# Kernel tuning notes

Hardware: AMD Instinct MI355X
Metric: run time of the kernel (lower is better)

The kernel has to match this reference:

```python
import jax, jax.numpy as jnp
import numpy as np

E = 8        # num_experts
K = 2        # top_k
LN_EPS = 1e-5

def setup_inputs() -> dict:
    key = jax.random.key(0)
    B, S, D, F = 4, 2048, 1024, 4096
    F2 = F // 2  # shared expert ffn_dim // 2
    ks = jax.random.split(key, 8)
    s = 0.02
    return {
        "hidden_states": jax.random.normal(ks[0], (B, S, D), jnp.float32),
        "router_w": jax.random.normal(ks[1], (D, E), jnp.float32) * s,
        "router_b": jnp.zeros((E,), jnp.float32),
        "w1": jax.random.normal(ks[2], (E, D, F), jnp.float32) * s,
        "b1": jnp.zeros((E, F), jnp.float32),
        "gate": jnp.ones((E, F), jnp.float32),          # specialization_gate per expert
        "w2": jax.random.normal(ks[3], (E, F, D), jnp.float32) * s,
        "b2": jnp.zeros((E, D), jnp.float32),
        "sw1": jax.random.normal(ks[4], (D, F2), jnp.float32) * s,
        "sb1": jnp.zeros((F2,), jnp.float32),
        "sgate": jnp.ones((F2,), jnp.float32),
        "sw2": jax.random.normal(ks[5], (F2, D), jnp.float32) * s,
        "sb2": jnp.zeros((D,), jnp.float32),
        "shared_weight": jnp.float32(0.5),
        "ln_g": jnp.ones((D,), jnp.float32),
        "ln_b": jnp.zeros((D,), jnp.float32),
    }


def _expert_ffn(x, w1, b1, gate, w2, b2):
    # fc1 -> specialization gate -> exact GELU -> fc2 (dropout is identity in eval)
    h = jax.nn.gelu((x @ w1 + b1) * gate, approximate=False)
    return h @ w2 + b2


def reference(hidden_states, router_w, router_b, w1, b1, gate, w2, b2,
              sw1, sb1, sgate, sw2, sb2, shared_weight, ln_g, ln_b):
    x = hidden_states  # [B,S,D]
    # --- router (eval: no noise, no capacity mask) ---
    logits = jnp.einsum('bsd,de->bse', x, router_w) + router_b
    probs = jax.nn.softmax(logits, axis=-1)                # [B,S,E]
    topk_p, topk_i = jax.lax.top_k(probs, K)               # [B,S,K]
    topk_p = topk_p / jnp.sum(topk_p, axis=-1, keepdims=True)
    # per-token per-expert combine weight: sum over k slots assigned to expert e
    combine = jnp.sum(jax.nn.one_hot(topk_i, E, dtype=x.dtype) * topk_p[..., None], axis=-2)  # [B,S,E]
    # --- expert dispatch/combine (dense equivalent; zero weight = no contribution) ---
    moe = jnp.zeros_like(x)
    for e in range(E):  # small fixed loop over experts
        moe = moe + combine[..., e:e + 1] * _expert_ffn(x, w1[e], b1[e], gate[e], w2[e], b2[e])
    # --- shared expert ---
    shared = _expert_ffn(x, sw1, sb1, sgate, sw2, sb2) * jax.nn.sigmoid(shared_weight)
    y = moe + shared
    # --- output LayerNorm ---
    mu = jnp.mean(y, axis=-1, keepdims=True)
    var = jnp.var(y, axis=-1, keepdims=True)
    return (y - mu) * jax.lax.rsqrt(var + LN_EPS) * ln_g + ln_b
```

## Files before the change

kernel.cpp:

```cpp
#include <hip/hip_runtime.h>
#include <hip/hip_bf16.h>
#include <stdint.h>

typedef __attribute__((ext_vector_type(8))) short bf16x8;
typedef __attribute__((ext_vector_type(4))) float f32x4;
typedef __attribute__((ext_vector_type(4))) unsigned short us4;

#define T_TOK 8192
#define DDIM 1024
#define FDIM 4096
#define F2DIM 2048
#define NEXP 8
#define NTPB1 4352
#define NRBLK 2048
#define FC1_T 5344

__device__ __forceinline__ unsigned short f2bf(float f) {
    unsigned u = __float_as_uint(f);
    u += 0x7fffu + ((u >> 16) & 1u);
    return (unsigned short)(u >> 16);
}
__device__ __forceinline__ float bf2f(unsigned short h) {
    return __uint_as_float(((unsigned)h) << 16);
}
__device__ __forceinline__ float gelu_fast(float v) {
    float u = 0.7978845608028654f * v * (1.0f + 0.044715f * v * v);
    float a = fabsf(u);
    float t = __expf(-2.0f * a);
    float th = (1.0f - t) / (1.0f + t);
    th = u < 0.0f ? -th : th;
    return 0.5f * v * (1.0f + th);
}

__device__ __forceinline__ void gl2lds16(const void* g, void* l) {
    __builtin_amdgcn_global_load_lds(
        (const __attribute__((address_space(1))) unsigned int*)(unsigned long long)g,
        (__attribute__((address_space(3))) unsigned int*)(unsigned int)(unsigned long long)l,
        16, 0, 0);
}

__device__ __forceinline__ void tp_block(const float* __restrict__ in,
                                         unsigned short* __restrict__ out,
                                         int Cin, long long ibase, int n0, int k0,
                                         long long unit0, float (*ts)[132], int tid) {
#pragma unroll
    for (int i = 0; i < 8; ++i) {
        int idx = tid + i * 256;
        int k = idx >> 5, t4 = idx & 31;
        float4 v = *(const float4*)(in + ibase + (long long)(k0 + k) * Cin + n0 + t4 * 4);
        *(float4*)&ts[k][t4 * 4] = v;
    }
    __syncthreads();
#pragma unroll
    for (int i = 0; i < 4; ++i) {
        int idx = tid + i * 256;
        int u = idx >> 9, cid = idx & 511;
        int row = cid >> 2, c = cid & 3;
        int gc = c ^ ((row >> 1) & 3);
        const int kb = u * 32 + gc * 8;
        us4 o0, o1;
        o0.x = f2bf(ts[kb + 0][row]); o0.y = f2bf(ts[kb + 1][row]);
        o0.z = f2bf(ts[kb + 2][row]); o0.w = f2bf(ts[kb + 3][row]);
        o1.x = f2bf(ts[kb + 4][row]); o1.y = f2bf(ts[kb + 5][row]);
        o1.z = f2bf(ts[kb + 6][row]); o1.w = f2bf(ts[kb + 7][row]);
        unsigned short* dst = out + (unit0 + u) * 4096 + (long long)cid * 8;
        *(us4*)dst = o0;
        *(us4*)(dst + 4) = o1;
    }
}

__global__ void k_prep1(const float* __restrict__ w1, const float* __restrict__ sw1,
                        unsigned short* __restrict__ w1t, unsigned short* __restrict__ sw1t,
                        const float* __restrict__ x, const float* __restrict__ rw,
                        const float* __restrict__ rbv, int* __restrict__ eid,
                        float* __restrict__ ewt, int* __restrict__ bcnt,
                        unsigned short* __restrict__ xb) {
    const int blk = blockIdx.x;
    const int tid = threadIdx.x;

    if (blk < NTPB1) {
        __shared__ float ts[64][132];
        if (blk < 4096) {
            int e = blk >> 9, l = blk & 511;
            int nb = l >> 4, ks = l & 15;
            tp_block(w1, w1t, 4096, (long long)e * 1024 * 4096,
                     nb * 128, ks * 64, (long long)e * 1024 + nb * 32 + ks * 2, ts, tid);
        } else {
            int l = blk - 4096;
            int nb = l >> 4, ks = l & 15;
            tp_block(sw1, sw1t, 2048, 0, nb * 128, ks * 64, nb * 32 + ks * 2, ts, tid);
        }
        return;
    }

    __shared__ int hcnt[8];
    const int rblk = blk - NTPB1;
    const int wid = tid >> 6, lane = tid & 63;
    const int t = rblk * 4 + wid;
    if (tid < 8) hcnt[tid] = 0;
    __syncthreads();

    float acc[8];
#pragma unroll
    for (int e = 0; e < 8; ++e) acc[e] = 0.f;
    const float4* xr = (const float4*)(x + (long long)t * DDIM);
#pragma unroll
    for (int c = 0; c < 4; ++c) {
        float4 xv = xr[lane + 64 * c];
        int d0 = (lane + 64 * c) * 4;
        us4 o;
        o.x = f2bf(xv.x); o.y = f2bf(xv.y); o.z = f2bf(xv.z); o.w = f2bf(xv.w);
        *(us4*)(xb + (long long)t * DDIM + d0) = o;
        float xs[4] = {xv.x, xv.y, xv.z, xv.w};
#pragma unroll
        for (int j = 0; j < 4; ++j) {
            const float* wrow = rw + (long long)(d0 + j) * 8;
#pragma unroll
            for (int e = 0; e < 8; ++e) acc[e] += xs[j] * wrow[e];
        }
    }
#pragma unroll
    for (int off = 32; off; off >>= 1)
#pragma unroll
        for (int e = 0; e < 8; ++e) acc[e] += __shfl_xor(acc[e], off);
    if (lane == 0) {
        float lg[8];
#pragma unroll
        for (int e = 0; e < 8; ++e) lg[e] = acc[e] + rbv[e];
        int e0 = 0;
#pragma unroll
        for (int e = 1; e < 8; ++e) if (lg[e] > lg[e0]) e0 = e;
        int e1 = -1;
#pragma unroll
        for (int e = 0; e < 8; ++e) {
            if (e == e0) continue;
            if (e1 < 0 || lg[e] > lg[e1]) e1 = e;
        }
        float w0 = 1.f / (1.f + expf(lg[e1] - lg[e0]));
        eid[2 * t] = e0; eid[2 * t + 1] = e1;
        ewt[2 * t] = w0; ewt[2 * t + 1] = 1.f - w0;
        atomicAdd(&hcnt[e0], 1);
        atomicAdd(&hcnt[e1], 1);
    }
    __syncthreads();
    if (tid < 8) bcnt[rblk * 8 + tid] = hcnt[tid];
}

__global__ void k_scan2(const int* __restrict__ bcnt, int* __restrict__ cnt,
                        int* __restrict__ offs, int* __restrict__ blkbase) {
    __shared__ int part[256];
    __shared__ int ctot[8];
    __shared__ int gbase[8];
    const int tid = threadIdx.x;
    const int e = tid >> 5, j = tid & 31;
    int s = 0;
    for (int r = j * 64; r < j * 64 + 64; ++r) s += bcnt[r * 8 + e];
    part[tid] = s;
    __syncthreads();
    if (j == 0) {
        int run = 0;
        for (int k = 0; k < 32; ++k) { int v = part[e * 32 + k]; part[e * 32 + k] = run; run += v; }
        ctot[e] = run;
    }
    __syncthreads();
    if (tid == 0) {
        int run = 0;
        for (int ee = 0; ee < NEXP; ++ee) {
            offs[ee] = run; cnt[ee] = ctot[ee]; gbase[ee] = run; run += ctot[ee];
        }
        offs[NEXP] = run;
    }
    __syncthreads();
    int run = gbase[e] + part[tid];
    for (int r = j * 64; r < j * 64 + 64; ++r) {
        blkbase[r * 8 + e] = run;
        run += bcnt[r * 8 + e];
    }
}

__global__ void k_scatter2(const int* __restrict__ eid, const float* __restrict__ ewt,
                           const int* __restrict__ blkbase, int* __restrict__ rowtok,
                           float* __restrict__ roww, int* __restrict__ pos) {
    const int t = blockIdx.x * 256 + threadIdx.x;
    const int rb = t >> 2;
    const int g = t & 3;
    const int lane = threadIdx.x & 63;
    const int lb = lane & ~3;
    int e0 = eid[2 * t], e1 = eid[2 * t + 1];
    int r0 = 0, r1 = 0;
#pragma unroll
    for (int q = 0; q < 4; ++q) {
        int oe0 = __shfl(e0, lb + q, 64);
        int oe1 = __shfl(e1, lb + q, 64);
        if (q < g) {
            r0 += (oe0 == e0) + (oe1 == e0);
            r1 += (oe0 == e1) + (oe1 == e1);
        }
    }
    int p0 = blkbase[rb * 8 + e0] + r0;
    int p1 = blkbase[rb * 8 + e1] + r1;
    rowtok[p0] = (t << 1);     roww[p0] = ewt[2 * t];     pos[2 * t] = p0;
    rowtok[p1] = (t << 1) | 1; roww[p1] = ewt[2 * t + 1]; pos[2 * t + 1] = p1;
}

template <int FC>
__launch_bounds__(256, 4)
__global__ void k_fc(const short* __restrict__ Amoe, const short* __restrict__ Ash,
                     const short* __restrict__ Bmoe, const short* __restrict__ Bsh,
                     const float* __restrict__ biasM, const float* __restrict__ biasS,
                     const float* __restrict__ gateM, const float* __restrict__ gateS,
                     unsigned short* __restrict__ outM, unsigned short* __restrict__ outS,
                     const int* __restrict__ cnt, const int* __restrict__ offs,
                     const int* __restrict__ rowtok, const float* __restrict__ roww,
                     const float* __restrict__ swp,
                     const float* __restrict__ w2raw, const float* __restrict__ sw2raw,
                     unsigned short* __restrict__ w2t_o, unsigned short* __restrict__ sw2t_o) {
    __shared__ __align__(16) char smem_raw[34816];

    if (FC == 1 && blockIdx.x >= FC1_T) {
        float (*ts)[132] = (float(*)[132])smem_raw;
        int tb = blockIdx.x - FC1_T;
        if (tb < 4096) {
            int e = tb >> 9, l = tb & 511;
            int nb = l >> 6, ks = l & 63;
            tp_block(w2raw, w2t_o, 1024, (long long)e * 4096 * 1024,
                     nb * 128, ks * 64, (long long)e * 1024 + nb * 128 + ks * 2,
                     ts, threadIdx.x);
        } else {
            int l = tb - 4096;
            int nb = l >> 5, ks = l & 31;
            tp_block(sw2raw, sw2t_o, 1024, 0, nb * 128, ks * 64,
                     nb * 64 + ks * 2, ts, threadIdx.x);
        }
        return;
    }

    int RBz[9];
    int T = 0;
#pragma unroll
    for (int zz = 0; zz < 9; ++zz) {
        int Mz = (zz < 8) ? cnt[zz] : T_TOK;
        int rbn = (Mz + 127) >> 7;
        int cbn = (FC == 1) ? ((zz < 8) ? 32 : 16) : 8;
        RBz[zz] = rbn;
        T += rbn * cbn;
    }
    const int ell = blockIdx.x;
    if (ell >= T) return;
    const int q = T >> 3, r = T & 7;
    const int xk = ell & 7, jj = ell >> 3;
    int t = (xk < r ? xk * (q + 1) : r * (q + 1) + (xk - r) * q) + jj;

    int z = 0, local = t;
    for (; z < 9; ++z) {
        int cbn = (FC == 1) ? ((z < 8) ? 32 : 16) : 8;
        int tz = RBz[z] * cbn;
        if (local < tz) break;
        local -= tz;
    }
    const int RB = RBz[z];
    int cb, rb;
    if (FC == 1) {
        cb = local / RB;
        rb = local - cb * RB;
    } else {
        rb = local >> 3;
        cb = local & 7;
    }

    const bool sh = (z == 8);
    const int Kd = (FC == 1) ? 1024 : (sh ? 2048 : 4096);
    const int Ncols = (FC == 1) ? (sh ? 2048 : 4096) : 1024;
    const int KB = Kd / 32;
    const int M = sh ? T_TOK : cnt[z];
    const int oE = sh ? 0 : offs[z];

    const short* A = sh ? Ash : Amoe;
    const short* B = sh ? Bsh : Bmoe + (long long)z * 4194304;

    short* Asb = (short*)smem_raw;
    short* Bsb = Asb + 8192;

    const int tid = threadIdx.x, w = tid >> 6, lane = tid & 63;
    const int fr = lane & 15, fg = lane >> 4;
    const int wr = w >> 1, wc = w & 1;

    const short *ag0, *ag1;
    {
        int id = tid, row = id >> 2;
        int gc = (id & 3) ^ ((row >> 1) & 3);
        int rA = rb * 128 + row; if (rA > M - 1) rA = M - 1;
        long long rowix;
        if (FC == 1) rowix = sh ? (long long)rA : (long long)(rowtok[oE + rA] >> 1);
        else         rowix = sh ? (long long)rA : (long long)(oE + rA);
        ag0 = A + rowix * (long long)Kd + gc * 8;
    }
    {
        int id = tid + 256, row = id >> 2;
        int gc = (id & 3) ^ ((row >> 1) & 3);
        int rA = rb * 128 + row; if (rA > M - 1) rA = M - 1;
        long long rowix;
        if (FC == 1) rowix = sh ? (long long)rA : (long long)(rowtok[oE + rA] >> 1);
        else         rowix = sh ? (long long)rA : (long long)(oE + rA);
        ag1 = A + rowix * (long long)Kd + gc * 8;
    }
    const short* bb = B + (long long)cb * KB * 4096 + (long long)tid * 8;

    short* const a0d0 = Asb + w * 512;
    short* const a0d1 = Asb + 2048 + w * 512;
    short* const a1d0 = Asb + 4096 + w * 512;
    short* const a1d1 = Asb + 4096 + 2048 + w * 512;
    short* const b0d0 = Bsb + w * 512;
    short* const b0d1 = Bsb + 2048 + w * 512;
    short* const b1d0 = Bsb + 4096 + w * 512;
    short* const b1d1 = Bsb + 4096 + 2048 + w * 512;

    f32x4 acc[4][4];
#pragma unroll
    for (int m = 0; m < 4; ++m)
#pragma unroll
        for (int n = 0; n < 4; ++n)
            acc[m][n] = (f32x4){0.f, 0.f, 0.f, 0.f};

    const int slot = fg ^ ((fr >> 1) & 3);
    const int arow0 = wr * 64 + fr;
    const int brow0 = wc * 64 + fr;
    const int nk = Kd / 64;

    for (int kt = 0; kt < nk; ++kt) {
        gl2lds16(ag0, a0d0);       gl2lds16(ag0 + 32, a1d0);
        gl2lds16(ag1, a0d1);       gl2lds16(ag1 + 32, a1d1);
        gl2lds16(bb, b0d0);        gl2lds16(bb + 2048, b0d1);
        gl2lds16(bb + 4096, b1d0); gl2lds16(bb + 6144, b1d1);
        ag0 += 64; ag1 += 64; bb += 8192;
        __syncthreads();

#pragma unroll
        for (int s = 0; s < 2; ++s) {
            bf16x8 a[4], b[4];
#pragma unroll
            for (int m = 0; m < 4; ++m)
                a[m] = *(const bf16x8*)(Asb + s * 4096 + (arow0 + m * 16) * 32 + slot * 8);
#pragma unroll
            for (int n = 0; n < 4; ++n)
                b[n] = *(const bf16x8*)(Bsb + s * 4096 + (brow0 + n * 16) * 32 + slot * 8);
#pragma unroll
            for (int m = 0; m < 4; ++m)
#pragma unroll
                for (int n = 0; n < 4; ++n)
                    acc[m][n] = __builtin_amdgcn_mfma_f32_16x16x32_bf16(a[m], b[n], acc[m][n], 0, 0, 0);
        }
        __syncthreads();
    }

    const int mrow0 = rb * 128 + wr * 64;
    const int col0 = cb * 128 + wc * 64;

    if (FC == 1) {
        const float* bp = sh ? biasS : biasM + (long long)z * FDIM;
        const float* gp = sh ? gateS : gateM + (long long)z * FDIM;
        unsigned short* outp = sh ? outS : outM;
        const long long obase = sh ? 0 : (long long)oE;
        float bv[4], gv[4]; int coln[4];
#pragma unroll
        for (int n = 0; n < 4; ++n) {
            coln[n] = col0 + n * 16 + fr;
            bv[n] = bp[coln[n]];
            gv[n] = gp[coln[n]];
        }
#pragma unroll
        for (int m = 0; m < 4; ++m) {
#pragma unroll
            for (int i = 0; i < 4; ++i) {
                int grow = mrow0 + m * 16 + fg * 4 + i;
                if (grow < M) {
                    unsigned short* rowp = outp + (obase + grow) * (long long)Ncols;
#pragma unroll
                    for (int n = 0; n < 4; ++n) {
                        float v = (acc[m][n][i] + bv[n]) * gv[n];
                        rowp[coln[n]] = f2bf(gelu_fast(v));
                    }
                }
            }
        }
    } else {
        float bv[4]; int coln[4];
        const float* bp = sh ? biasS : biasM + (long long)z * DDIM;
#pragma unroll
        for (int n = 0; n < 4; ++n) {
            coln[n] = col0 + n * 16 + fr;
            bv[n] = bp[coln[n]];
        }
        if (sh) {
            float sigw = 1.f / (1.f + expf(-swp[0]));
#pragma unroll
            for (int m = 0; m < 4; ++m) {
#pragma unroll
                for (int i = 0; i < 4; ++i) {
                    int grow = mrow0 + m * 16 + fg * 4 + i;
                    if (grow < M) {
                        unsigned short* rowp = outS + (long long)grow * DDIM;
#pragma unroll
                        for (int n = 0; n < 4; ++n)
                            rowp[coln[n]] = f2bf((acc[m][n][i] + bv[n]) * sigw);
                    }
                }
            }
        } else {
#pragma unroll
            for (int m = 0; m < 4; ++m) {
#pragma unroll
                for (int i = 0; i < 4; ++i) {
                    int grow = mrow0 + m * 16 + fg * 4 + i;
                    if (grow < M) {
                        int p = oE + grow;
                        float wv = roww[p];
                        unsigned short* rowp = outM + (long long)p * DDIM;
#pragma unroll
                        for (int n = 0; n < 4; ++n)
                            rowp[coln[n]] = f2bf((acc[m][n][i] + bv[n]) * wv);
                    }
                }
            }
        }
    }
}

__global__ void k_ln(const unsigned short* __restrict__ yc,
                     const unsigned short* __restrict__ ysh,
                     const int* __restrict__ pos,
                     const float* __restrict__ g, const float* __restrict__ b,
                     float* __restrict__ out) {
    const int wid = threadIdx.x >> 6, lane = threadIdx.x & 63;
    const long long t = (long long)blockIdx.x * 4 + wid;
    const long long b0 = (long long)pos[2 * t] * DDIM;
    const long long b1 = (long long)pos[2 * t + 1] * DDIM;
    const long long bs = t * DDIM;
    float v[16];
    float s = 0.f, sq = 0.f;
#pragma unroll
    for (int j = 0; j < 2; ++j) {
        int c0 = (lane + 64 * j) * 8;
        uint4 a0 = *(const uint4*)(yc + b0 + c0);
        uint4 a1 = *(const uint4*)(yc + b1 + c0);
        uint4 a2 = *(const uint4*)(ysh + bs + c0);
        const unsigned* u0 = (const unsigned*)&a0;
        const unsigned* u1 = (const unsigned*)&a1;
        const unsigned* u2 = (const unsigned*)&a2;
#pragma unroll
        for (int qq = 0; qq < 4; ++qq) {
            float lo = bf2f((unsigned short)u0[qq]) + bf2f((unsigned short)u1[qq]) +
                       bf2f((unsigned short)u2[qq]);
            float hi = bf2f((unsigned short)(u0[qq] >> 16)) + bf2f((unsigned short)(u1[qq] >> 16)) +
                       bf2f((unsigned short)(u2[qq] >> 16));
            v[j * 8 + qq * 2] = lo;
            v[j * 8 + qq * 2 + 1] = hi;
            s += lo + hi;
            sq += lo * lo + hi * hi;
        }
    }
#pragma unroll
    for (int off = 32; off; off >>= 1) {
        s += __shfl_xor(s, off);
        sq += __shfl_xor(sq, off);
    }
    const float mean = s * (1.f / DDIM);
    const float var = sq * (1.f / DDIM) - mean * mean;
    const float inv = rsqrtf(var + 1e-5f);
#pragma unroll
    for (int j = 0; j < 2; ++j) {
        int c0 = (lane + 64 * j) * 8;
#pragma unroll
        for (int h = 0; h < 2; ++h) {
            float4 o4;
            float* op = (float*)&o4;
#pragma unroll
            for (int qq = 0; qq < 4; ++qq) {
                int k = h * 4 + qq;
                int col = c0 + k;
                op[qq] = (v[j * 8 + k] - mean) * inv * g[col] + b[col];
            }
            *(float4*)(out + bs + c0 + h * 4) = o4;
        }
    }
}

extern "C" void kernel_launch(void* const* d_in, const int* in_sizes, int n_in,
                              void* d_out, int out_size, void* d_ws, size_t ws_size,
                              hipStream_t stream) {
    const float* x    = (const float*)d_in[0];
    const float* rw   = (const float*)d_in[1];
    const float* rb   = (const float*)d_in[2];
    const float* w1   = (const float*)d_in[3];
    const float* b1   = (const float*)d_in[4];
    const float* gate = (const float*)d_in[5];
    const float* w2   = (const float*)d_in[6];
    const float* b2   = (const float*)d_in[7];
    const float* sw1  = (const float*)d_in[8];
    const float* sb1  = (const float*)d_in[9];
    const float* sgate= (const float*)d_in[10];
    const float* sw2  = (const float*)d_in[11];
    const float* sb2  = (const float*)d_in[12];
    const float* swt  = (const float*)d_in[13];
    const float* lng  = (const float*)d_in[14];
    const float* lnb  = (const float*)d_in[15];
    float* out = (float*)d_out;

    char* p = (char*)d_ws;
    auto take = [&](size_t n) { char* r = p; p += (n + 255) & ~(size_t)255; return r; };
    short* xb   = (short*)take((size_t)T_TOK * DDIM * 2);
    short* w1t  = (short*)take((size_t)NEXP * FDIM * DDIM * 2);
    short* w2t  = (short*)take((size_t)NEXP * DDIM * FDIM * 2);
    short* sw1t = (short*)take((size_t)F2DIM * DDIM * 2);
    short* sw2t = (short*)take((size_t)DDIM * F2DIM * 2);
    short* hbuf = (short*)take((size_t)2 * T_TOK * FDIM * 2);
    short* hs   = (short*)take((size_t)T_TOK * F2DIM * 2);
    unsigned short* ycomp = (unsigned short*)take((size_t)2 * T_TOK * DDIM * 2);
    unsigned short* ysh   = (unsigned short*)take((size_t)T_TOK * DDIM * 2);
    int* eid    = (int*)take((size_t)T_TOK * 2 * 4);
    float* ewt  = (float*)take((size_t)T_TOK * 2 * 4);
    int* rowtok = (int*)take((size_t)2 * T_TOK * 4);
    float* roww = (float*)take((size_t)2 * T_TOK * 4);
    int* pos    = (int*)take((size_t)2 * T_TOK * 4);
    int* bcnt   = (int*)take((size_t)NRBLK * 8 * 4);
    int* blkbase= (int*)take((size_t)NRBLK * 8 * 4);
    int* cnt    = (int*)take(64);
    int* offs   = (int*)take(64);

    k_prep1<<<NTPB1 + NRBLK, 256, 0, stream>>>(
        w1, sw1, (unsigned short*)w1t, (unsigned short*)sw1t,
        x, rw, rb, eid, ewt, bcnt, (unsigned short*)xb);

    k_scan2<<<1, 256, 0, stream>>>(bcnt, cnt, offs, blkbase);
    k_scatter2<<<T_TOK / 256, 256, 0, stream>>>(eid, ewt, blkbase, rowtok, roww, pos);

    k_fc<1><<<FC1_T + 4096 + 256, 256, 0, stream>>>(
        xb, xb, w1t, sw1t, b1, sb1, gate, sgate,
        (unsigned short*)hbuf, (unsigned short*)hs, cnt, offs, rowtok, roww, swt,
        w2, sw2, (unsigned short*)w2t, (unsigned short*)sw2t);
    k_fc<2><<<1592, 256, 0, stream>>>(
        hbuf, hs, w2t, sw2t, b2, sb2, (const float*)nullptr, (const float*)nullptr,
        ycomp, ysh, cnt, offs, rowtok, roww, swt,
        (const float*)nullptr, (const float*)nullptr,
        (unsigned short*)nullptr, (unsigned short*)nullptr);

    k_ln<<<T_TOK / 4, 256, 0, stream>>>(ycomp, ysh, pos, lng, lnb, out);
}
```

Baseline: 590.6 us.

## Fuse routing scan and scatter into one kernel; regroup FC1 tile order

Merges the single-block scan kernel and the scatter kernel into one 32-block routing kernel. Each block redoes the per-expert partial sums and keeps its per-row-block bases in shared memory instead of a global blkbase array. This removes one launch and a global round trip, at the cost of redundant scan work in every block. Separately, FC1 tile indices are regrouped so four adjacent column blocks share a row block, which is meant to improve L2 reuse of A rows.

```diff
diff --git a/kernel.cpp b/kernel.cpp
--- a/kernel.cpp
+++ b/kernel.cpp
@@ -146,59 +146,63 @@
     if (tid < 8) bcnt[rblk * 8 + tid] = hcnt[tid];
 }
 
-__global__ void k_scan2(const int* __restrict__ bcnt, int* __restrict__ cnt,
-                        int* __restrict__ offs, int* __restrict__ blkbase) {
-    __shared__ int part[256];
+__global__ void k_route(const int* __restrict__ bcnt, const int* __restrict__ eid,
+                        const float* __restrict__ ewt, int* __restrict__ cnt,
+                        int* __restrict__ offs, int* __restrict__ rowtok,
+                        float* __restrict__ roww, int* __restrict__ pos) {
+    __shared__ int part[8][33];
     __shared__ int ctot[8];
     __shared__ int gbase[8];
+    __shared__ int lb[64][8];
     const int tid = threadIdx.x;
     const int e = tid >> 5, j = tid & 31;
     int s = 0;
     for (int r = j * 64; r < j * 64 + 64; ++r) s += bcnt[r * 8 + e];
-    part[tid] = s;
+    part[e][j] = s;
     __syncthreads();
     if (j == 0) {
         int run = 0;
-        for (int k = 0; k < 32; ++k) { int v = part[e * 32 + k]; part[e * 32 + k] = run; run += v; }
+        for (int k = 0; k < 32; ++k) { int v = part[e][k]; part[e][k] = run; run += v; }
         ctot[e] = run;
     }
     __syncthreads();
     if (tid == 0) {
         int run = 0;
-        for (int ee = 0; ee < NEXP; ++ee) {
-            offs[ee] = run; cnt[ee] = ctot[ee]; gbase[ee] = run; run += ctot[ee];
-        }
-        offs[NEXP] = run;
-    }
-    __syncthreads();
-    int run = gbase[e] + part[tid];
-    for (int r = j * 64; r < j * 64 + 64; ++r) {
-        blkbase[r * 8 + e] = run;
-        run += bcnt[r * 8 + e];
-    }
-}
-
-__global__ void k_scatter2(const int* __restrict__ eid, const float* __restrict__ ewt,
-                           const int* __restrict__ blkbase, int* __restrict__ rowtok,
-                           float* __restrict__ roww, int* __restrict__ pos) {
-    const int t = blockIdx.x * 256 + threadIdx.x;
-    const int rb = t >> 2;
+        for (int ee = 0; ee < NEXP; ++ee) { gbase[ee] = run; run += ctot[ee]; }
+        if (blockIdx.x == 0) {
+            int r2 = 0;
+            for (int ee = 0; ee < NEXP; ++ee) { offs[ee] = r2; cnt[ee] = ctot[ee]; r2 += ctot[ee]; }
+            offs[NEXP] = r2;
+        }
+    }
+    __syncthreads();
+    if (tid < 8) {
+        int ee = tid;
+        int run = gbase[ee] + part[ee][blockIdx.x];
+        int r0 = blockIdx.x * 64;
+        for (int r = 0; r < 64; ++r) {
+            lb[r][ee] = run;
+            run += bcnt[(r0 + r) * 8 + ee];
+        }
+    }
+    __syncthreads();
+    const int t = blockIdx.x * 256 + tid;
+    const int rloc = tid >> 2;
     const int g = t & 3;
-    const int lane = threadIdx.x & 63;
-    const int lb = lane & ~3;
+    const int lane = tid & 63, lbn = lane & ~3;
     int e0 = eid[2 * t], e1 = eid[2 * t + 1];
     int r0 = 0, r1 = 0;
 #pragma unroll
     for (int q = 0; q < 4; ++q) {
-        int oe0 = __shfl(e0, lb + q, 64);
-        int oe1 = __shfl(e1, lb + q, 64);
+        int oe0 = __shfl(e0, lbn + q, 64);
+        int oe1 = __shfl(e1, lbn + q, 64);
         if (q < g) {
             r0 += (oe0 == e0) + (oe1 == e0);
             r1 += (oe0 == e1) + (oe1 == e1);
         }
     }
-    int p0 = blkbase[rb * 8 + e0] + r0;
-    int p1 = blkbase[rb * 8 + e1] + r1;
+    int p0 = lb[rloc][e0] + r0;
+    int p1 = lb[rloc][e1] + r1;
     rowtok[p0] = (t << 1);     roww[p0] = ewt[2 * t];     pos[2 * t] = p0;
     rowtok[p1] = (t << 1) | 1; roww[p1] = ewt[2 * t + 1]; pos[2 * t + 1] = p1;
 }
@@ -261,8 +265,11 @@
     const int RB = RBz[z];
     int cb, rb;
     if (FC == 1) {
-        cb = local / RB;
-        rb = local - cb * RB;
+        int grp = RB * 4;
+        int cbg = local / grp;
+        int r2 = local - cbg * grp;
+        rb = r2 >> 2;
+        cb = cbg * 4 + (r2 & 3);
     } else {
         rb = local >> 3;
         cb = local & 7;
@@ -523,7 +530,6 @@
     float* roww = (float*)take((size_t)2 * T_TOK * 4);
     int* pos    = (int*)take((size_t)2 * T_TOK * 4);
     int* bcnt   = (int*)take((size_t)NRBLK * 8 * 4);
-    int* blkbase= (int*)take((size_t)NRBLK * 8 * 4);
     int* cnt    = (int*)take(64);
     int* offs   = (int*)take(64);
 
@@ -531,8 +537,7 @@
         w1, sw1, (unsigned short*)w1t, (unsigned short*)sw1t,
         x, rw, rb, eid, ewt, bcnt, (unsigned short*)xb);
 
-    k_scan2<<<1, 256, 0, stream>>>(bcnt, cnt, offs, blkbase);
-    k_scatter2<<<T_TOK / 256, 256, 0, stream>>>(eid, ewt, blkbase, rowtok, roww, pos);
+    k_route<<<32, 256, 0, stream>>>(bcnt, eid, ewt, cnt, offs, rowtok, roww, pos);
 
     k_fc<1><<<FC1_T + 4096 + 256, 256, 0, stream>>>(
         xb, xb, w1t, sw1t, b1, sb1, gate, sgate,
```

Result: faster. 572.2 us (-3.1%).
